# Kernel optimization log

Hardware: AMD Instinct MI355X
Metric: run time of the kernel (lower is better)

## Reference

```python
import jax, jax.numpy as jnp
import numpy as np

QUERY_DIM = 1024
KEY_DIM = 1024
NUM_HEADS = 16
HEAD_DIM = QUERY_DIM // NUM_HEADS


def setup_inputs() -> dict:
    key = jax.random.key(0)
    ks = jax.random.split(key, 11)
    B, Sq, Sk = 2, 2048, 2048
    s = 0.02
    return {
        "q": jax.random.normal(ks[0], (B, Sq, QUERY_DIM), jnp.float32),
        "k": jax.random.normal(ks[1], (B, Sk, KEY_DIM), jnp.float32),
        "v": jax.random.normal(ks[2], (B, Sk, KEY_DIM), jnp.float32),
        "Wq": jax.random.normal(ks[3], (QUERY_DIM, QUERY_DIM), jnp.float32) * s,
        "bq": jnp.zeros((QUERY_DIM,), jnp.float32),
        "Wk": jax.random.normal(ks[4], (KEY_DIM, QUERY_DIM), jnp.float32) * s,
        "bk": jnp.zeros((QUERY_DIM,), jnp.float32),
        "Wv": jax.random.normal(ks[5], (KEY_DIM, QUERY_DIM), jnp.float32) * s,
        "bv": jnp.zeros((QUERY_DIM,), jnp.float32),
        "Wo": jax.random.normal(ks[6], (QUERY_DIM, QUERY_DIM), jnp.float32) * s,
        "bo": jnp.zeros((QUERY_DIM,), jnp.float32),
    }


def reference(q, k, v, Wq, bq, Wk, bk, Wv, bv, Wo, bo):
    B, Sq, _ = q.shape
    Sk = k.shape[1]
    scale = HEAD_DIM ** -0.5
    # projections -> [B, H, S, Dh]
    qh = (q @ Wq + bq).reshape(B, Sq, NUM_HEADS, HEAD_DIM).transpose(0, 2, 1, 3)
    kh = (k @ Wk + bk).reshape(B, Sk, NUM_HEADS, HEAD_DIM).transpose(0, 2, 1, 3)
    vh = (v @ Wv + bv).reshape(B, Sk, NUM_HEADS, HEAD_DIM).transpose(0, 2, 1, 3)
    scores = jnp.einsum("bhqd,bhkd->bhqk", qh, kh) * scale
    attn = jax.nn.softmax(scores, axis=-1)
    out = jnp.einsum("bhqk,bhkd->bhqd", attn, vh)
    out = out.transpose(0, 2, 1, 3).reshape(B, Sq, QUERY_DIM)
    return out @ Wo + bo  # dropout is identity at inference
```

## Files before the change

kernel.cpp:

```cpp
#include <hip/hip_runtime.h>
#include <hip/hip_fp16.h>
#include <cstddef>


#define B_   2
#define S_   2048
#define D_   1024
#define H_   16
#define DH_  64

typedef _Float16 half8 __attribute__((ext_vector_type(8)));
typedef _Float16 half4 __attribute__((ext_vector_type(4)));
typedef float floatx4 __attribute__((ext_vector_type(4)));
typedef float floatx16 __attribute__((ext_vector_type(16)));
typedef int intx4 __attribute__((ext_vector_type(4)));

#define MFMA32(a, b, c) __builtin_amdgcn_mfma_f32_16x16x32_f16((a), (b), (c), 0, 0, 0)
#define MFMA3216(a, b, c) __builtin_amdgcn_mfma_f32_32x32x16_f16((a), (b), (c), 0, 0, 0)

__device__ __forceinline__ void half_swap(int& a, int& b, const int hi) {
#if __has_builtin(__builtin_amdgcn_permlane32_swap)
    (void)hi;
    auto r = __builtin_amdgcn_permlane32_swap(a, b, false, false);
    a = r[0]; b = r[1];
#else
    const int ax = __shfl_xor(a, 32, 64), bx = __shfl_xor(b, 32, 64);
    const int na = hi ? bx : a;
    b = hi ? b : ax;
    a = na;
#endif
}

__global__ __launch_bounds__(256) void prep(
    const float* __restrict__ q, const float* __restrict__ k,
    const float* __restrict__ v,
    __half* __restrict__ qf, __half* __restrict__ kf, __half* __restrict__ vf,
    const float* __restrict__ Wq, const float* __restrict__ Wk,
    const float* __restrict__ Wv, const float* __restrict__ Wo,
    __half* __restrict__ Wtq, __half* __restrict__ Wtk,
    __half* __restrict__ Wtv, __half* __restrict__ Wto)
{
    __shared__ __align__(16) __half T[64][72];
    const int tid = threadIdx.x;
    const int z = blockIdx.z;
    if (z < 3) {
        const float* srcs[3] = {q, k, v};
        __half* dsts[3] = {qf, kf, vf};
        const int i = blockIdx.x * 256 + tid;
        const float4* s = (const float4*)srcs[z];
        const float4 a = s[2 * i], b = s[2 * i + 1];
        half8 h;
        h[0] = (_Float16)a.x; h[1] = (_Float16)a.y; h[2] = (_Float16)a.z; h[3] = (_Float16)a.w;
        h[4] = (_Float16)b.x; h[5] = (_Float16)b.y; h[6] = (_Float16)b.z; h[7] = (_Float16)b.w;
        *(half8*)&dsts[z][(size_t)i * 8] = h;
        return;
    }
    if (blockIdx.x >= 256) return;
    const float* Ws[4] = {Wq, Wk, Wv, Wo};
    __half* Wts[4] = {Wtq, Wtk, Wtv, Wto};
    const int n0 = (blockIdx.x & 15) * 64, k0 = (blockIdx.x >> 4) * 64;
    for (int w = 0; w < 4; ++w) {
        const float* W = Ws[w];
        __half* Wt = Wts[w];
        #pragma unroll
        for (int p = 0; p < 4; ++p) {
            const int c = tid + p * 256;
            const int kr = c >> 4, nc = (c & 15) * 4;
            const float4 a = *(const float4*)&W[(size_t)(k0 + kr) * D_ + n0 + nc];
            T[nc + 0][kr] = __float2half(a.x);
            T[nc + 1][kr] = __float2half(a.y);
            T[nc + 2][kr] = __float2half(a.z);
            T[nc + 3][kr] = __float2half(a.w);
        }
        __syncthreads();
        #pragma unroll
        for (int p = 0; p < 2; ++p) {
            const int c = tid + p * 256;
            const int nr = c >> 3, kc = (c & 7) * 8;
            *(half8*)&Wt[(size_t)(n0 + nr) * D_ + k0 + kc] = *(const half8*)&T[nr][kc];
        }
        __syncthreads();
    }
}

__device__ __forceinline__ void gemm_core(
    const __half* __restrict__ A, const __half* __restrict__ Bt,
    const float* __restrict__ bias, void* __restrict__ dst,
    const int mode, const float oscale)
{
    __shared__ __align__(16) char gsm[36864];
    __half (*As)[72] = (__half(*)[72])gsm;
    __half (*Bs)[72] = (__half(*)[72])(gsm + 18432);

    const int tid = threadIdx.x;
    const int m0 = blockIdx.y * 128, n0 = blockIdx.x * 128;
    const int lane = tid & 63, wv = tid >> 6;
    const int quad = lane >> 4, lr = lane & 15;
    const int wm0 = (wv >> 1) * 64, wn0 = (wv & 1) * 64;

    floatx4 acc[4][4];
    #pragma unroll
    for (int i = 0; i < 4; ++i)
        #pragma unroll
        for (int j = 0; j < 4; ++j)
            acc[i][j] = (floatx4){0.f, 0.f, 0.f, 0.f};

    half8 pa[4], pb[4];
    #pragma unroll
    for (int p = 0; p < 4; ++p) {
        const int c = tid + p * 256;
        const int row = c >> 3, seg = (c & 7) * 8;
        pa[p] = *(const half8*)&A [(size_t)(m0 + row) * D_ + seg];
        pb[p] = *(const half8*)&Bt[(size_t)(n0 + row) * D_ + seg];
    }

    for (int k0 = 0; k0 < D_; k0 += 64) {
        __syncthreads();
        #pragma unroll
        for (int p = 0; p < 4; ++p) {
            const int c = tid + p * 256;
            const int row = c >> 3, seg = (c & 7) * 8;
            *(half8*)&As[row][seg] = pa[p];
            *(half8*)&Bs[row][seg] = pb[p];
        }
        if (k0 + 64 < D_) {
            #pragma unroll
            for (int p = 0; p < 4; ++p) {
                const int c = tid + p * 256;
                const int row = c >> 3, seg = (c & 7) * 8;
                pa[p] = *(const half8*)&A [(size_t)(m0 + row) * D_ + k0 + 64 + seg];
                pb[p] = *(const half8*)&Bt[(size_t)(n0 + row) * D_ + k0 + 64 + seg];
            }
        }
        __syncthreads();
        #pragma unroll
        for (int ks = 0; ks < 2; ++ks) {
            const int ko = quad * 8 + ks * 32;
            half8 af[4], bf[4];
            #pragma unroll
            for (int i = 0; i < 4; ++i) af[i] = *(const half8*)&As[wm0 + i * 16 + lr][ko];
            #pragma unroll
            for (int j = 0; j < 4; ++j) bf[j] = *(const half8*)&Bs[wn0 + j * 16 + lr][ko];
            #pragma unroll
            for (int i = 0; i < 4; ++i)
                #pragma unroll
                for (int j = 0; j < 4; ++j)
                    acc[i][j] = MFMA32(af[i], bf[j], acc[i][j]);
        }
    }

    if (mode == 1) {
        float* out = (float*)dst;
        #pragma unroll
        for (int i = 0; i < 4; ++i) {
            #pragma unroll
            for (int j = 0; j < 4; ++j) {
                const int col = n0 + wn0 + j * 16 + lr;
                const float bval = bias[col];
                #pragma unroll
                for (int r = 0; r < 4; ++r) {
                    const int m = m0 + wm0 + i * 16 + quad * 4 + r;
                    out[(size_t)m * D_ + col] = acc[i][j][r] + bval;
                }
            }
        }
        return;
    }

    __syncthreads();
    __half (*Ct)[136] = (__half(*)[136])gsm;
    #pragma unroll
    for (int i = 0; i < 4; ++i) {
        #pragma unroll
        for (int j = 0; j < 4; ++j) {
            const int nl = wn0 + j * 16 + lr;
            const float bval = bias[n0 + nl];
            #pragma unroll
            for (int r = 0; r < 4; ++r) {
                const int ml = wm0 + i * 16 + quad * 4 + r;
                const _Float16 hv = (_Float16)((acc[i][j][r] + bval) * oscale);
                if (mode == 0) Ct[ml][nl] = hv;
                else           Ct[nl][ml] = hv;
            }
        }
    }
    __syncthreads();
    __half* oh = (__half*)dst;
    #pragma unroll
    for (int p = 0; p < 8; ++p) {
        const int row = (tid >> 4) + p * 16;
        const int cs  = (tid & 15) * 8;
        const half8 vls = *(const half8*)&Ct[row][cs];
        if (mode == 0) {
            const int m = m0 + row, col = n0 + cs;
            const int b = m >> 11, s = m & (S_ - 1);
            const int h = col >> 6, d = col & 63;
            *(half8*)&oh[(((size_t)(b * H_ + h) * S_ + s) << 6) + d] = vls;
        } else {
            const int col = n0 + row, m = m0 + cs;
            const int b = m >> 11, s = m & (S_ - 1);
            const int h = col >> 6, d = col & 63;
            *(half8*)&oh[((size_t)(b * H_ + h) * DH_ + d) * S_ + s] = vls;
        }
    }
}

__global__ __launch_bounds__(256) void gemm_proj(
    const __half* __restrict__ qf, const __half* __restrict__ kf,
    const __half* __restrict__ vf,
    const __half* __restrict__ Wtq, const __half* __restrict__ Wtk,
    const __half* __restrict__ Wtv,
    const float* __restrict__ bq, const float* __restrict__ bk,
    const float* __restrict__ bv,
    __half* __restrict__ qhf, __half* __restrict__ khf, __half* __restrict__ vht)
{
    const __half* As[3] = {qf, kf, vf};
    const __half* Bts[3] = {Wtq, Wtk, Wtv};
    const float* bs[3] = {bq, bk, bv};
    __half* ds[3] = {qhf, khf, vht};
    const int z = blockIdx.z;
    gemm_core(As[z], Bts[z], bs[z], ds[z], z == 2 ? 2 : 0,
              z == 0 ? 0.1803368801111244f : 1.0f);
}

__global__ __launch_bounds__(256) void gemm_final(
    const __half* __restrict__ attf, const __half* __restrict__ Wto,
    const float* __restrict__ bo, float* __restrict__ out)
{
    gemm_core(attf, Wto, bo, out, 1, 1.0f);
}

__global__ __launch_bounds__(256, 4) void attn_f16(
    const __half* __restrict__ qhf, const __half* __restrict__ khf,
    const __half* __restrict__ vht, __half* __restrict__ attf)
{
    __shared__ __align__(16) char smem[36864];

    const int tid = threadIdx.x;
    const int lane = tid & 63, wv = tid >> 6;
    const int l31 = lane & 31, hi = lane >> 5;
    const int kb = wv >> 1, qb = wv & 1;
    const int bh = blockIdx.y;
    const int q0 = blockIdx.x * 64;
    const size_t hbase = (size_t)bh * S_ * DH_;

    half8 qB[4];
    #pragma unroll
    for (int ds = 0; ds < 4; ++ds)
        qB[ds] = *(const half8*)&qhf[hbase
            + (size_t)(q0 + qb * 32 + l31) * DH_ + ds * 16 + hi * 8];

    float lp = 0.f;
    floatx16 O[2];
    #pragma unroll
    for (int i = 0; i < 16; ++i) { O[0][i] = 0.f; O[1][i] = 0.f; }

    {
        __half (*K0)[72] = (__half(*)[72])smem;
        __half (*V0)[72] = (__half(*)[72])(smem + 9216);
        #pragma unroll
        for (int p = 0; p < 2; ++p) {
            const int c = tid + p * 256;
            const int row = c >> 3, seg = (c & 7) * 8;
            *(half8*)&K0[row][seg] = *(const half8*)&khf[hbase + (size_t)row * DH_ + seg];
            *(half8*)&V0[row][seg] = *(const half8*)&vht[hbase + (size_t)row * S_ + seg];
        }
    }
    half8 pk[2], pv[2];
    #pragma unroll
    for (int p = 0; p < 2; ++p) {
        const int c = tid + p * 256;
        const int row = c >> 3, seg = (c & 7) * 8;
        pk[p] = *(const half8*)&khf[hbase + (size_t)(64 + row) * DH_ + seg];
        pv[p] = *(const half8*)&vht[hbase + (size_t)row * S_ + 64 + seg];
    }
    __syncthreads();

    for (int kt = 0; kt < S_; kt += 64) {
        const int cb = (kt >> 6) & 1;
        __half (*Ks)[72] = (__half(*)[72])(smem + cb * 18432);
        __half (*Vs)[72] = (__half(*)[72])(smem + cb * 18432 + 9216);
        __half (*Kn)[72] = (__half(*)[72])(smem + (cb ^ 1) * 18432);
        __half (*Vn)[72] = (__half(*)[72])(smem + (cb ^ 1) * 18432 + 9216);

        if (kt + 64 < S_) {
            #pragma unroll
            for (int p = 0; p < 2; ++p) {
                const int c = tid + p * 256;
                const int row = c >> 3, seg = (c & 7) * 8;
                *(half8*)&Kn[row][seg] = pk[p];
                *(half8*)&Vn[row][seg] = pv[p];
            }
            if (kt + 128 < S_) {
                #pragma unroll
                for (int p = 0; p < 2; ++p) {
                    const int c = tid + p * 256;
                    const int row = c >> 3, seg = (c & 7) * 8;
                    pk[p] = *(const half8*)&khf[hbase + (size_t)(kt + 128 + row) * DH_ + seg];
                    pv[p] = *(const half8*)&vht[hbase + (size_t)row * S_ + kt + 128 + seg];
                }
            }
        }

        floatx16 s;
        #pragma unroll
        for (int i = 0; i < 16; ++i) s[i] = 0.f;
        __builtin_amdgcn_s_setprio(1);
        #pragma unroll
        for (int ds = 0; ds < 4; ++ds) {
            const half8 aK = *(const half8*)&Ks[kb * 32 + l31][ds * 16 + hi * 8];
            s = MFMA3216(aK, qB[ds], s);
        }
        __builtin_amdgcn_s_setprio(0);

        #pragma unroll
        for (int r = 0; r < 16; ++r) {
            const float e = __builtin_amdgcn_exp2f(s[r]);
            lp += e;
            s[r] = e;
        }

        half8 pB[2];
        #pragma unroll
        for (int ks = 0; ks < 2; ++ks) {
            int P0 = __builtin_bit_cast(int, __builtin_amdgcn_cvt_pkrtz(s[ks * 8 + 0], s[ks * 8 + 1]));
            int P1 = __builtin_bit_cast(int, __builtin_amdgcn_cvt_pkrtz(s[ks * 8 + 2], s[ks * 8 + 3]));
            int P2 = __builtin_bit_cast(int, __builtin_amdgcn_cvt_pkrtz(s[ks * 8 + 4], s[ks * 8 + 5]));
            int P3 = __builtin_bit_cast(int, __builtin_amdgcn_cvt_pkrtz(s[ks * 8 + 6], s[ks * 8 + 7]));
            half_swap(P0, P2, hi);
            half_swap(P1, P3, hi);
            const intx4 w = {P0, P1, P2, P3};
            pB[ks] = __builtin_bit_cast(half8, w);
        }

        __builtin_amdgcn_s_setprio(1);
        #pragma unroll
        for (int db = 0; db < 2; ++db)
            #pragma unroll
            for (int ks = 0; ks < 2; ++ks) {
                const half8 aV = *(const half8*)&Vs[db * 32 + l31][kb * 32 + ks * 16 + hi * 8];
                O[db] = MFMA3216(aV, pB[ks], O[db]);
            }
        __builtin_amdgcn_s_setprio(0);

        __syncthreads();
    }

    float (*R)[68] = (float(*)[68])smem;
    __half (*F)[72] = (__half(*)[72])(smem + 17408);
    float* Lred = (float*)(smem + 26624);

    lp += __shfl_xor(lp, 32, 64);
    if (lane < 32) Lred[kb * 64 + qb * 32 + l31] = lp;
    if (kb == 1) {
        #pragma unroll
        for (int db = 0; db < 2; ++db)
            #pragma unroll
            for (int r = 0; r < 16; ++r) {
                const int d = db * 32 + (r & 3) + 8 * (r >> 2) + 4 * hi;
                R[d][qb * 32 + l31] = O[db][r];
            }
    }
    __syncthreads();
    if (kb == 0) {
        const int qg = qb * 32 + l31;
        const float il = 1.0f / (Lred[qg] + Lred[64 + qg]);
        #pragma unroll
        for (int db = 0; db < 2; ++db)
            #pragma unroll
            for (int r = 0; r < 16; ++r) {
                const int d = db * 32 + (r & 3) + 8 * (r >> 2) + 4 * hi;
                F[qg][d] = __float2half((O[db][r] + R[d][qg]) * il);
            }
    }
    __syncthreads();

    const int b = bh >> 4, h = bh & 15;
    const int qrow = tid >> 2, dseg = (tid & 3) * 16;
    __half* dstp = &attf[(((size_t)(b * S_ + q0 + qrow)) << 10) + h * DH_ + dseg];
    *(half8*)&dstp[0] = *(const half8*)&F[qrow][dseg];
    *(half8*)&dstp[8] = *(const half8*)&F[qrow][dseg + 8];
}

extern "C" void kernel_launch(void* const* d_in, const int* in_sizes, int n_in,
                              void* d_out, int out_size, void* d_ws, size_t ws_size,
                              hipStream_t stream) {
    const float* q  = (const float*)d_in[0];
    const float* k  = (const float*)d_in[1];
    const float* v  = (const float*)d_in[2];
    const float* Wq = (const float*)d_in[3];
    const float* bq = (const float*)d_in[4];
    const float* Wk = (const float*)d_in[5];
    const float* bk = (const float*)d_in[6];
    const float* Wv = (const float*)d_in[7];
    const float* bv = (const float*)d_in[8];
    const float* Wo = (const float*)d_in[9];
    const float* bo = (const float*)d_in[10];
    float* out = (float*)d_out;

    __half* ws = (__half*)d_ws;
    const size_t NE = (size_t)B_ * S_ * D_;
    __half* qf   = ws;
    __half* kf   = ws + NE;
    __half* vf   = ws + 2 * NE;
    __half* qhf  = ws + 3 * NE;
    __half* khf  = ws + 4 * NE;
    __half* vht  = ws + 5 * NE;
    __half* attf = ws + 6 * NE;
    __half* Wtq  = ws + 7 * NE;
    __half* Wtk  = Wtq + (size_t)D_ * D_;
    __half* Wtv  = Wtk + (size_t)D_ * D_;
    __half* Wto  = Wtv + (size_t)D_ * D_;

    const dim3 blk(256);
    prep<<<dim3((unsigned)(NE / 8 / 256), 1, 4), blk, 0, stream>>>(
        q, k, v, qf, kf, vf, Wq, Wk, Wv, Wo, Wtq, Wtk, Wtv, Wto);

    gemm_proj<<<dim3(D_ / 128, (B_ * S_) / 128, 3), blk, 0, stream>>>(
        qf, kf, vf, Wtq, Wtk, Wtv, bq, bk, bv, qhf, khf, vht);

    attn_f16<<<dim3(S_ / 64, B_ * H_), blk, 0, stream>>>(qhf, khf, vht, attf);

    gemm_final<<<dim3(D_ / 128, (B_ * S_) / 128), blk, 0, stream>>>(attf, Wto, bo, out);
}
```

Before: 229.6 us.

## Widen attention blocks to 128 queries and compute row sums with fdot2

The attention kernel now uses 512-thread blocks of eight waves covering 128 query rows. Each K/V tile staged in shared memory is shared by twice as many queries, the grid is halved, and each thread stages a single half8 per tile using pointer increments. Softmax row sums come from packed fp16 dot products against ones (fdot2), which replaces the per-element float adds. The epilogue writes normalized outputs as half4 vectors through a reused shared buffer. The risks are higher register pressure under the 512-thread launch bound, fewer blocks in flight, and row sums accumulated from fp16-rounded probabilities.

```diff
diff --git a/kernel.cpp b/kernel.cpp
--- a/kernel.cpp
+++ b/kernel.cpp
@@ -11,12 +11,19 @@
 
 typedef _Float16 half8 __attribute__((ext_vector_type(8)));
 typedef _Float16 half4 __attribute__((ext_vector_type(4)));
+typedef _Float16 half2v __attribute__((ext_vector_type(2)));
 typedef float floatx4 __attribute__((ext_vector_type(4)));
 typedef float floatx16 __attribute__((ext_vector_type(16)));
 typedef int intx4 __attribute__((ext_vector_type(4)));
 
 #define MFMA32(a, b, c) __builtin_amdgcn_mfma_f32_16x16x32_f16((a), (b), (c), 0, 0, 0)
 #define MFMA3216(a, b, c) __builtin_amdgcn_mfma_f32_32x32x16_f16((a), (b), (c), 0, 0, 0)
+
+#if __has_builtin(__builtin_amdgcn_fdot2)
+#define LP_FDOT2 1
+#else
+#define LP_FDOT2 0
+#endif
 
 __device__ __forceinline__ void half_swap(int& a, int& b, const int hi) {
 #if __has_builtin(__builtin_amdgcn_permlane32_swap)
@@ -230,7 +237,7 @@
     gemm_core(attf, Wto, bo, out, 1, 1.0f);
 }
 
-__global__ __launch_bounds__(256, 4) void attn_f16(
+__global__ __launch_bounds__(512, 4) void attn_f16(
     const __half* __restrict__ qhf, const __half* __restrict__ khf,
     const __half* __restrict__ vht, __half* __restrict__ attf)
 {
@@ -239,9 +246,9 @@
     const int tid = threadIdx.x;
     const int lane = tid & 63, wv = tid >> 6;
     const int l31 = lane & 31, hi = lane >> 5;
-    const int kb = wv >> 1, qb = wv & 1;
+    const int kb = wv >> 2, qb = wv & 3;
     const int bh = blockIdx.y;
-    const int q0 = blockIdx.x * 64;
+    const int q0 = blockIdx.x * 128;
     const size_t hbase = (size_t)bh * S_ * DH_;
 
     half8 qB[4];
@@ -250,31 +257,30 @@
         qB[ds] = *(const half8*)&qhf[hbase
             + (size_t)(q0 + qb * 32 + l31) * DH_ + ds * 16 + hi * 8];
 
-    float lp = 0.f;
+    float lp0 = 0.f, lp1 = 0.f;
+#if !LP_FDOT2
+    float lp2 = 0.f, lp3 = 0.f;
+#endif
     floatx16 O[2];
     #pragma unroll
     for (int i = 0; i < 16; ++i) { O[0][i] = 0.f; O[1][i] = 0.f; }
+
+    const int srow = tid >> 3, sseg = (tid & 7) * 8;
+    const __half* kg = khf + hbase + (size_t)srow * DH_ + sseg;
+    const __half* vg = vht + hbase + (size_t)srow * S_ + sseg;
 
     {
         __half (*K0)[72] = (__half(*)[72])smem;
         __half (*V0)[72] = (__half(*)[72])(smem + 9216);
-        #pragma unroll
-        for (int p = 0; p < 2; ++p) {
-            const int c = tid + p * 256;
-            const int row = c >> 3, seg = (c & 7) * 8;
-            *(half8*)&K0[row][seg] = *(const half8*)&khf[hbase + (size_t)row * DH_ + seg];
-            *(half8*)&V0[row][seg] = *(const half8*)&vht[hbase + (size_t)row * S_ + seg];
-        }
-    }
-    half8 pk[2], pv[2];
-    #pragma unroll
-    for (int p = 0; p < 2; ++p) {
-        const int c = tid + p * 256;
-        const int row = c >> 3, seg = (c & 7) * 8;
-        pk[p] = *(const half8*)&khf[hbase + (size_t)(64 + row) * DH_ + seg];
-        pv[p] = *(const half8*)&vht[hbase + (size_t)row * S_ + 64 + seg];
-    }
-    __syncthreads();
+        *(half8*)&K0[srow][sseg] = *(const half8*)kg;
+        *(half8*)&V0[srow][sseg] = *(const half8*)vg;
+    }
+    kg += 64 * DH_; vg += 64;
+    half8 pk = *(const half8*)kg;
+    half8 pv = *(const half8*)vg;
+    __syncthreads();
+
+    const half2v one2 = {(_Float16)1.0f, (_Float16)1.0f};
 
     for (int kt = 0; kt < S_; kt += 64) {
         const int cb = (kt >> 6) & 1;
@@ -284,21 +290,12 @@
         __half (*Vn)[72] = (__half(*)[72])(smem + (cb ^ 1) * 18432 + 9216);
 
         if (kt + 64 < S_) {
-            #pragma unroll
-            for (int p = 0; p < 2; ++p) {
-                const int c = tid + p * 256;
-                const int row = c >> 3, seg = (c & 7) * 8;
-                *(half8*)&Kn[row][seg] = pk[p];
-                *(half8*)&Vn[row][seg] = pv[p];
-            }
+            *(half8*)&Kn[srow][sseg] = pk;
+            *(half8*)&Vn[srow][sseg] = pv;
             if (kt + 128 < S_) {
-                #pragma unroll
-                for (int p = 0; p < 2; ++p) {
-                    const int c = tid + p * 256;
-                    const int row = c >> 3, seg = (c & 7) * 8;
-                    pk[p] = *(const half8*)&khf[hbase + (size_t)(kt + 128 + row) * DH_ + seg];
-                    pv[p] = *(const half8*)&vht[hbase + (size_t)row * S_ + kt + 128 + seg];
-                }
+                kg += 64 * DH_; vg += 64;
+                pk = *(const half8*)kg;
+                pv = *(const half8*)vg;
             }
         }
 
@@ -316,11 +313,15 @@
         #pragma unroll
         for (int r = 0; r < 16; ++r) {
             const float e = __builtin_amdgcn_exp2f(s[r]);
-            lp += e;
+#if !LP_FDOT2
+            (r & 2) ? ((r & 1) ? (lp3 += e) : (lp2 += e))
+                    : ((r & 1) ? (lp1 += e) : (lp0 += e));
+#endif
             s[r] = e;
         }
 
         half8 pB[2];
+        int PW[2][4];
         #pragma unroll
         for (int ks = 0; ks < 2; ++ks) {
             int P0 = __builtin_bit_cast(int, __builtin_amdgcn_cvt_pkrtz(s[ks * 8 + 0], s[ks * 8 + 1]));
@@ -329,6 +330,7 @@
             int P3 = __builtin_bit_cast(int, __builtin_amdgcn_cvt_pkrtz(s[ks * 8 + 6], s[ks * 8 + 7]));
             half_swap(P0, P2, hi);
             half_swap(P1, P3, hi);
+            PW[ks][0] = P0; PW[ks][1] = P1; PW[ks][2] = P2; PW[ks][3] = P3;
             const intx4 w = {P0, P1, P2, P3};
             pB[ks] = __builtin_bit_cast(half8, w);
         }
@@ -343,34 +345,61 @@
             }
         __builtin_amdgcn_s_setprio(0);
 
+#if LP_FDOT2
+        #pragma unroll
+        for (int ks = 0; ks < 2; ++ks) {
+            lp0 = __builtin_amdgcn_fdot2(__builtin_bit_cast(half2v, PW[ks][0]), one2, lp0, false);
+            lp1 = __builtin_amdgcn_fdot2(__builtin_bit_cast(half2v, PW[ks][1]), one2, lp1, false);
+            lp0 = __builtin_amdgcn_fdot2(__builtin_bit_cast(half2v, PW[ks][2]), one2, lp0, false);
+            lp1 = __builtin_amdgcn_fdot2(__builtin_bit_cast(half2v, PW[ks][3]), one2, lp1, false);
+        }
+#endif
+
         __syncthreads();
     }
 
-    float (*R)[68] = (float(*)[68])smem;
-    __half (*F)[72] = (__half(*)[72])(smem + 17408);
-    float* Lred = (float*)(smem + 26624);
-
+    float (*R)[132] = (float(*)[132])smem;
+    float* Lred = (float*)(smem + 33792);
+
+#if LP_FDOT2
+    float lp = lp0 + lp1;
+#else
+    float lp = (lp0 + lp1) + (lp2 + lp3);
+#endif
     lp += __shfl_xor(lp, 32, 64);
-    if (lane < 32) Lred[kb * 64 + qb * 32 + l31] = lp;
+    const int qg = qb * 32 + l31;
+    if (lane < 32) Lred[kb * 128 + qg] = lp;
     if (kb == 1) {
         #pragma unroll
         for (int db = 0; db < 2; ++db)
             #pragma unroll
             for (int r = 0; r < 16; ++r) {
                 const int d = db * 32 + (r & 3) + 8 * (r >> 2) + 4 * hi;
-                R[d][qb * 32 + l31] = O[db][r];
+                R[d][qg] = O[db][r];
             }
     }
     __syncthreads();
     if (kb == 0) {
-        const int qg = qb * 32 + l31;
-        const float il = 1.0f / (Lred[qg] + Lred[64 + qg]);
+        const float il = 1.0f / (Lred[qg] + Lred[128 + qg]);
         #pragma unroll
         for (int db = 0; db < 2; ++db)
             #pragma unroll
             for (int r = 0; r < 16; ++r) {
                 const int d = db * 32 + (r & 3) + 8 * (r >> 2) + 4 * hi;
-                F[qg][d] = __float2half((O[db][r] + R[d][qg]) * il);
+                O[db][r] = (O[db][r] + R[d][qg]) * il;
+            }
+    }
+    __syncthreads();
+    __half (*F)[72] = (__half(*)[72])smem;
+    if (kb == 0) {
+        #pragma unroll
+        for (int db = 0; db < 2; ++db)
+            #pragma unroll
+            for (int t = 0; t < 4; ++t) {
+                half4 hv;
+                #pragma unroll
+                for (int r = 0; r < 4; ++r) hv[r] = (_Float16)O[db][t * 4 + r];
+                *(half4*)&F[qg][db * 32 + t * 8 + hi * 4] = hv;
             }
     }
     __syncthreads();
@@ -419,7 +448,7 @@
     gemm_proj<<<dim3(D_ / 128, (B_ * S_) / 128, 3), blk, 0, stream>>>(
         qf, kf, vf, Wtq, Wtk, Wtv, bq, bk, bv, qhf, khf, vht);
 
-    attn_f16<<<dim3(S_ / 64, B_ * H_), blk, 0, stream>>>(qhf, khf, vht, attf);
+    attn_f16<<<dim3(S_ / 128, B_ * H_), dim3(512), 0, stream>>>(qhf, khf, vht, attf);
 
     gemm_final<<<dim3(D_ / 128, (B_ * S_) / 128), blk, 0, stream>>>(attf, Wto, bo, out);
 }
```

New measurement: 225.1 us. 2.0% less time.
